# Optimization experiments

Hardware: AMD Instinct MI355X
Metric: run time of the kernel (lower is better)

## Reference

```python
import jax, jax.numpy as jnp
import numpy as np

KH, KW = 3, 3
PAD, STRIDE = 1, 1
KD = 3  # depth kernel extent; extended with one zero slice -> 4 indices


def _unfold(x, pad, stride):
    # x: (B, C, H, W) -> (B, C, KH*KW, oH, oW), patches ordered row-major like F.unfold
    B, C, H, W = x.shape
    xp = jnp.pad(x, ((0, 0), (0, 0), (pad, pad), (pad, pad)))
    oH = (H + 2 * pad - KH) // stride + 1
    oW = (W + 2 * pad - KW) // stride + 1
    pats = [xp[:, :, i:i + (oH - 1) * stride + 1:stride, j:j + (oW - 1) * stride + 1:stride]
            for i in range(KH) for j in range(KW)]
    return jnp.stack(pats, axis=2)


def setup_inputs() -> dict:
    key = jax.random.key(0)
    k1, k2, k3 = jax.random.split(key, 3)
    features = jax.random.normal(k1, (4, 16, 512, 512), dtype=jnp.float32)
    depth = jax.random.randint(k2, (4, 512, 512), 0, 8, dtype=jnp.int32)
    weight = jax.random.normal(k3, (32, 16, 3, 3, 3), dtype=jnp.float32) * 0.05
    return {"features": features, "depth": depth, "weight": weight}


def reference(features, depth, weight):
    oC, iC = weight.shape[0], weight.shape[1]
    # unfolded input patches: (B, iC, 9, oH, oW)
    patches = _unfold(features, PAD, STRIDE)
    # unfolded depth: (B, 9, oH, oW); padding fills with depth 0 (matches F.unfold)
    dpat = _unfold(depth[:, None, :, :].astype(jnp.int32), PAD, STRIDE)[:, 0]
    center = dpat[:, KH * KW // 2][:, None]  # (B, 1, oH, oW)
    diff = dpat - center
    # diff < -1 or diff >= 1 -> select appended zero slice (index 3); else diff+1
    idx = jnp.where((diff < -1) | (diff >= 1), 3, diff + 1)  # (B, 9, oH, oW) in [0, 3]
    onehot = jax.nn.one_hot(idx, KD + 1, dtype=features.dtype)  # (B, 9, oH, oW, 4)
    # extended weight with zero depth-slice: (oC, iC, 4, 9)
    ext_w = jnp.concatenate([weight, jnp.zeros_like(weight[:, :, :1])], axis=2)
    ext_w = ext_w.reshape(oC, iC, KD + 1, KH * KW)
    # per-pixel depth-gated 3x3x3 conv (bias is never added in the original op)
    out = jnp.einsum('oidk,bkhwd,bikhw->bohw', ext_w, onehot, patches)
    return out
```

## Files before the change

kernel.cpp:

```cpp
#include <hip/hip_runtime.h>
#include <hip/hip_bf16.h>


#define IC 16
#define OC 32
#define Hh 512
#define Ww 512
#define HW (Hh * Ww)
#define TW 256
#define TR 2
#define NT 4
#define SENTu 0x1000
#define PY  514
#define PXF 514
#define PXD 516
#define FTP_BYTES (4ull * PY * PXF * IC * 2)

typedef __attribute__((ext_vector_type(8))) short short8;
typedef __attribute__((ext_vector_type(4))) float float4v;
typedef __attribute__((ext_vector_type(2))) unsigned int uint2v;
typedef __attribute__((ext_vector_type(4))) unsigned int uint4v;

__device__ __forceinline__ unsigned short f2bf(float x) {
    unsigned u = __float_as_uint(x);
    unsigned r = u + 0x7FFFu + ((u >> 16) & 1u);
    return (unsigned short)(r >> 16);
}
__device__ __forceinline__ unsigned packbf(float a, float b) {
    union { __hip_bfloat162 h2; unsigned u; } cv;
    cv.h2 = __float22bfloat162_rn(make_float2(a, b));
    return cv.u;
}
__device__ __forceinline__ void gl16(const void* g, void* l) {
    __builtin_amdgcn_global_load_lds(
        (const __attribute__((address_space(1))) unsigned int*)g,
        (__attribute__((address_space(3))) unsigned int*)l, 16, 0, 0);
}
__device__ __forceinline__ void gl4(const void* g, void* l) {
    __builtin_amdgcn_global_load_lds(
        (const __attribute__((address_space(1))) unsigned int*)g,
        (__attribute__((address_space(3))) unsigned int*)l, 4, 0, 0);
}

__global__ void prep_weights(const float* __restrict__ wgt,
                             unsigned short* __restrict__ wsA) {
    int e = blockIdx.x * 256 + threadIdx.x;
    if (e >= 9 * 2 * 64 * 8) return;
    int j    = e & 7;
    int lane = (e >> 3) & 63;
    int mt   = (e >> 9) & 1;
    int c    = e >> 10;
    int oc = mt * 16 + (lane & 15);
    int kk = ((lane >> 4) << 3) + j;
    wsA[e] = f2bf(wgt[oc * 432 + (kk >> 1) * 27 + (kk & 1) * 9 + c]);
}

__global__ __launch_bounds__(256) void prep_feat(const float* __restrict__ feat,
                                                 unsigned short* __restrict__ ftp) {
    const int e  = blockIdx.x * 256 + threadIdx.x;
    const int xq = e & 127;
    const int y  = (e >> 7) & 511;
    const int b  = e >> 16;
    float4v v[16];
    const float* fb = feat + ((size_t)(b * IC) << 18) + (y << 9) + (xq << 2);
#pragma unroll
    for (int ic = 0; ic < IC; ++ic)
        v[ic] = *(const float4v*)(fb + ((size_t)ic << 18));
#pragma unroll
    for (int i = 0; i < 4; ++i) {
        const int xp = (xq << 2) + i + 1;
        const int q  = (xp >> 2) & 3;
        unsigned pk[8];
#pragma unroll
        for (int j = 0; j < 8; ++j)
            pk[j] = packbf(v[2 * j][i], v[2 * j + 1][i]);
        uint2v c0 = {pk[0], pk[1]}, c1 = {pk[2], pk[3]},
               c2 = {pk[4], pk[5]}, c3 = {pk[6], pk[7]};
        if (q & 1) { uint2v t = c0; c0 = c1; c1 = t; t = c2; c2 = c3; c3 = t; }
        if (q & 2) { uint2v t = c0; c0 = c2; c2 = t; t = c1; c1 = c3; c3 = t; }
        uint4v* dst = (uint4v*)(ftp + (((size_t)b * PY + (y + 1)) * PXF + xp) * 16);
        dst[0] = (uint4v){c0.x, c0.y, c1.x, c1.y};
        dst[1] = (uint4v){c2.x, c2.y, c3.x, c3.y};
    }
}

__global__ __launch_bounds__(256) void prep_depth(const int* __restrict__ depth,
                                                  unsigned short* __restrict__ dpad) {
    const int e = blockIdx.x * 256 + threadIdx.x;
    if (e >= 4 * PY * PXD) return;
    const int xp = e % PXD;
    const int yb = e / PXD;
    const int yp = yb % PY;
    const int b  = yb / PY;
    unsigned short v = (unsigned short)SENTu;
    const int xi = xp - 1, yi = yp - 1;
    if ((unsigned)xi < (unsigned)Ww && (unsigned)yi < (unsigned)Hh)
        v = (unsigned short)depth[(b << 18) + (yi << 9) + xi];
    dpad[e] = v;
}

__global__ __launch_bounds__(512, 2) void depconv_main(
    const unsigned short* __restrict__ ftp,
    const unsigned short* __restrict__ dpad,
    const unsigned short* __restrict__ wsA,
    float* __restrict__ out)
{
    __shared__ alignas(16) unsigned short ftile[2][TR + 2][258][16];
    __shared__ alignas(16) unsigned short dtile[2][TR + 2][260];

    const int tid = threadIdx.x;
    const int bid = blockIdx.x;
    const int wg  = (bid & 7) * 64 + (bid >> 3);
    const int t0  = wg * NT;

    const int lane = tid & 63;
    const int wv   = tid >> 6;
    const int g    = lane >> 4;
    const int n    = lane & 15;
    const int rr   = wv >> 2;
    const int xoff = (wv & 3) * 64;
    const int qs   = lane >> 4;
    const int oc0  = lane & 15;

    short8 wfrag[9][2];
    {
        const short8* ap = (const short8*)wsA;
#pragma unroll
        for (int c = 0; c < 9; ++c) {
            wfrag[c][0] = ap[(c * 2 + 0) * 64 + lane];
            wfrag[c][1] = ap[(c * 2 + 1) * 64 + lane];
        }
    }

    auto stageF = [&](int p, int tt) {
        const int b = tt >> 9, rowblk = (tt >> 1) & 255, colblk = tt & 1;
        const int h0 = rowblk * TR, wstart = colblk * TW;
        const char* gbase = (const char*)(ftp + (((size_t)b * PY + h0) * PXF + wstart) * 16);
#pragma unroll
        for (int r = 0; r < TR + 2; ++r) {
            const char* rg = gbase + (size_t)r * (PXF * 32);
            char* lr = (char*)&ftile[p][r][0][0];
            gl16(rg + tid * 16,      lr + wv * 1024);
            gl16(rg + 64 + tid * 16, lr + 64 + wv * 1024);
        }
    };
    auto stageD = [&](int p, int tt) {
        const int b = tt >> 9, rowblk = (tt >> 1) & 255, colblk = tt & 1;
        const int h0 = rowblk * TR, wstart = colblk * TW;
        const char* gb = (const char*)(dpad + ((size_t)b * PY + h0) * PXD + wstart);
        char* lb = (char*)&dtile[p][0][0];
#pragma unroll
        for (int pass = 0; pass < 2; ++pass) {
            const unsigned off = pass ? 32u : 0u;
            const unsigned d   = off + tid * 4;
            const unsigned row = d / 520u;
            const unsigned col = d - row * 520u;
            gl4(gb + (size_t)row * (PXD * 2) + col, lb + off + wv * 256);
        }
    };

    auto compute = [&](int p, int tt) {
        const int b = tt >> 9, rowblk = (tt >> 1) & 255, colblk = tt & 1;
        const int h0 = rowblk * TR, wstart = colblk * TW;
        const int h = h0 + rr;
        float* opb0 = out + ((size_t)(b * OC + oc0) << 18) + ((size_t)h << 9);
#pragma unroll 1
        for (int it = 0; it < 4; ++it) {
            const int xb = xoff + it * 16 + n;
            const int dc = (int)dtile[p][rr + 1][xb + 1];
            float4v acc0 = {0.f, 0.f, 0.f, 0.f};
            float4v acc1 = {0.f, 0.f, 0.f, 0.f};
#pragma unroll
            for (int t = 0; t < 9; ++t) {
                const int kh = t / 3, kw = t % 3;
                const int px = xb + kw;
                unsigned mm;
                if (t == 4) {
                    mm = 0xffff0000u;
                } else {
                    const int diff = (int)dtile[p][rr + kh][px] - dc;
                    mm = (diff == 0) ? 0xffff0000u : ((diff == -1) ? 0x0000ffffu : 0u);
                }
                const int slot = (g ^ ((px >> 2) & 3)) << 2;
                const uint2v pr = *(const uint2v*)(&ftile[p][rr + kh][px][slot]);
                union { short8 s; unsigned u[4]; } bf;
                bf.u[0] = __builtin_amdgcn_perm(0u, pr.x, 0x01000100u) & mm;
                bf.u[1] = __builtin_amdgcn_perm(0u, pr.x, 0x03020302u) & mm;
                bf.u[2] = __builtin_amdgcn_perm(0u, pr.y, 0x01000100u) & mm;
                bf.u[3] = __builtin_amdgcn_perm(0u, pr.y, 0x03020302u) & mm;

                acc0 = __builtin_amdgcn_mfma_f32_16x16x32_bf16(bf.s, wfrag[t][0], acc0, 0, 0, 0);
                acc1 = __builtin_amdgcn_mfma_f32_16x16x32_bf16(bf.s, wfrag[t][1], acc1, 0, 0, 0);
            }
            const int w16 = wstart + xoff + it * 16;
            float* op = opb0 + (w16 + 4 * qs);
            *(float4v*)op                      = acc0;
            *(float4v*)(op + ((size_t)16 << 18)) = acc1;
        }
    };

    stageF(0, t0);
    stageD(0, t0);
    __syncthreads();
#pragma unroll 1
    for (int i = 0; i < NT; ++i) {
        const int p = i & 1;
        if (i + 1 < NT) {
            stageF(p ^ 1, t0 + i + 1);
            stageD(p ^ 1, t0 + i + 1);
        }
        compute(p, t0 + i);
        __syncthreads();
    }
}

extern "C" void kernel_launch(void* const* d_in, const int* in_sizes, int n_in,
                              void* d_out, int out_size, void* d_ws, size_t ws_size,
                              hipStream_t stream) {
    const float* feat  = (const float*)d_in[0];
    const int*   depth = (const int*)d_in[1];
    const float* wgt   = (const float*)d_in[2];
    float* out = (float*)d_out;

    unsigned short* wsA  = (unsigned short*)d_ws;
    unsigned short* ftp  = (unsigned short*)((char*)d_ws + 32768);
    unsigned short* dpad = (unsigned short*)((char*)d_ws + 32768 + FTP_BYTES);

    prep_weights<<<36, 256, 0, stream>>>(wgt, wsA);
    prep_feat<<<1024, 256, 0, stream>>>(feat, ftp);
    prep_depth<<<(4 * PY * PXD + 255) / 256, 256, 0, stream>>>(depth, dpad);
    depconv_main<<<512, 512, 0, stream>>>(ftp, dpad, wsA, out);
}
```

Baseline: 256.3 us.

## Give each wave private LDS buffers with waitcnt pipelining; merge weight and depth prep

The main conv kernel now has each wave own a private double-buffered LDS strip (4 rows by 64+2 columns). Waves prefetch their next x-group with global_load_lds and wait with explicit vmcnt counters instead of block-wide __syncthreads. The grid shrinks to 256 blocks at occupancy 1, and each wave processes four 64-wide column groups of a row pair. The weight and depth prep kernels are merged into one launch to cut launch overhead. The change trades inter-wave halo sharing, which means more redundant global loads per tile, and the lower occupancy for removing block barriers.

```diff
diff --git a/kernel.cpp b/kernel.cpp
--- a/kernel.cpp
+++ b/kernel.cpp
@@ -7,14 +7,14 @@
 #define Hh 512
 #define Ww 512
 #define HW (Hh * Ww)
-#define TW 256
-#define TR 2
-#define NT 4
 #define SENTu 0x1000
 #define PY  514
 #define PXF 514
 #define PXD 516
 #define FTP_BYTES (4ull * PY * PXF * IC * 2)
+#define WTW 64
+#define FROWB 2112
+#define DROWB 256
 
 typedef __attribute__((ext_vector_type(8))) short short8;
 typedef __attribute__((ext_vector_type(4))) float float4v;
@@ -42,17 +42,34 @@
         (__attribute__((address_space(3))) unsigned int*)l, 4, 0, 0);
 }
 
-__global__ void prep_weights(const float* __restrict__ wgt,
-                             unsigned short* __restrict__ wsA) {
-    int e = blockIdx.x * 256 + threadIdx.x;
-    if (e >= 9 * 2 * 64 * 8) return;
-    int j    = e & 7;
-    int lane = (e >> 3) & 63;
-    int mt   = (e >> 9) & 1;
-    int c    = e >> 10;
-    int oc = mt * 16 + (lane & 15);
-    int kk = ((lane >> 4) << 3) + j;
-    wsA[e] = f2bf(wgt[oc * 432 + (kk >> 1) * 27 + (kk & 1) * 9 + c]);
+__global__ __launch_bounds__(256) void prep_misc(const float* __restrict__ wgt,
+                                                 const int* __restrict__ depth,
+                                                 unsigned short* __restrict__ wsA,
+                                                 unsigned short* __restrict__ dpad) {
+    const int bid = blockIdx.x;
+    if (bid < 36) {
+        int e = bid * 256 + threadIdx.x;
+        if (e >= 9 * 2 * 64 * 8) return;
+        int j    = e & 7;
+        int lane = (e >> 3) & 63;
+        int mt   = (e >> 9) & 1;
+        int c    = e >> 10;
+        int oc = mt * 16 + (lane & 15);
+        int kk = ((lane >> 4) << 3) + j;
+        wsA[e] = f2bf(wgt[oc * 432 + (kk >> 1) * 27 + (kk & 1) * 9 + c]);
+    } else {
+        int e = (bid - 36) * 256 + threadIdx.x;
+        if (e >= 4 * PY * PXD) return;
+        const int xp = e % PXD;
+        const int yb = e / PXD;
+        const int yp = yb % PY;
+        const int b  = yb / PY;
+        unsigned short v = (unsigned short)SENTu;
+        const int xi = xp - 1, yi = yp - 1;
+        if ((unsigned)xi < (unsigned)Ww && (unsigned)yi < (unsigned)Hh)
+            v = (unsigned short)depth[(b << 18) + (yi << 9) + xi];
+        dpad[e] = v;
+    }
 }
 
 __global__ __launch_bounds__(256) void prep_feat(const float* __restrict__ feat,
@@ -84,43 +101,29 @@
     }
 }
 
-__global__ __launch_bounds__(256) void prep_depth(const int* __restrict__ depth,
-                                                  unsigned short* __restrict__ dpad) {
-    const int e = blockIdx.x * 256 + threadIdx.x;
-    if (e >= 4 * PY * PXD) return;
-    const int xp = e % PXD;
-    const int yb = e / PXD;
-    const int yp = yb % PY;
-    const int b  = yb / PY;
-    unsigned short v = (unsigned short)SENTu;
-    const int xi = xp - 1, yi = yp - 1;
-    if ((unsigned)xi < (unsigned)Ww && (unsigned)yi < (unsigned)Hh)
-        v = (unsigned short)depth[(b << 18) + (yi << 9) + xi];
-    dpad[e] = v;
-}
-
-__global__ __launch_bounds__(512, 2) void depconv_main(
+__global__ __launch_bounds__(512, 1) void depconv_main(
     const unsigned short* __restrict__ ftp,
     const unsigned short* __restrict__ dpad,
     const unsigned short* __restrict__ wsA,
     float* __restrict__ out)
 {
-    __shared__ alignas(16) unsigned short ftile[2][TR + 2][258][16];
-    __shared__ alignas(16) unsigned short dtile[2][TR + 2][260];
-
-    const int tid = threadIdx.x;
-    const int bid = blockIdx.x;
-    const int wg  = (bid & 7) * 64 + (bid >> 3);
-    const int t0  = wg * NT;
-
+    __shared__ alignas(16) char fbuf[8][2][4 * FROWB];
+    __shared__ alignas(16) char dbuf[8][2][4 * DROWB];
+
+    const int tid  = threadIdx.x;
     const int lane = tid & 63;
     const int wv   = tid >> 6;
-    const int g    = lane >> 4;
-    const int n    = lane & 15;
-    const int rr   = wv >> 2;
-    const int xoff = (wv & 3) * 64;
-    const int qs   = lane >> 4;
-    const int oc0  = lane & 15;
+    const int bid  = blockIdx.x;
+    const int wgb  = (bid & 7) * 32 + (bid >> 3);
+    const int widG = wgb * 8 + wv;
+    const int rp   = widG >> 1;
+    const int b    = rp >> 8;
+    const int rowpair = rp & 255;
+    const int xg0  = (widG & 1) * 4;
+    const int h0p  = rowpair * 2;
+
+    const int g = lane >> 4, n = lane & 15;
+    const int qs = lane >> 4, oc0 = lane & 15;
 
     short8 wfrag[9][2];
     {
@@ -132,86 +135,85 @@
         }
     }
 
-    auto stageF = [&](int p, int tt) {
-        const int b = tt >> 9, rowblk = (tt >> 1) & 255, colblk = tt & 1;
-        const int h0 = rowblk * TR, wstart = colblk * TW;
-        const char* gbase = (const char*)(ftp + (((size_t)b * PY + h0) * PXF + wstart) * 16);
-#pragma unroll
-        for (int r = 0; r < TR + 2; ++r) {
-            const char* rg = gbase + (size_t)r * (PXF * 32);
-            char* lr = (char*)&ftile[p][r][0][0];
-            gl16(rg + tid * 16,      lr + wv * 1024);
-            gl16(rg + 64 + tid * 16, lr + 64 + wv * 1024);
+    char* fb[2] = {fbuf[wv][0], fbuf[wv][1]};
+    char* db[2] = {dbuf[wv][0], dbuf[wv][1]};
+
+    auto issue = [&](char* fB, char* dB, int xg) {
+        const int wx0 = xg * WTW;
+        const char* gf = (const char*)ftp + (((size_t)b * PY + h0p) * PXF + wx0) * 32;
+        const char* gd = (const char*)dpad + (((size_t)b * PY + h0p) * PXD + wx0) * 2;
+#pragma unroll
+        for (int r = 0; r < 4; ++r) {
+            const char* rg = gf + (size_t)r * (PXF * 32);
+            char* lr = fB + r * FROWB;
+            gl16(rg + lane * 16,        lr);
+            gl16(rg + 1024 + lane * 16, lr + 1024);
+            gl4 (rg + 1856 + lane * 4,  lr + 1856);
+            gl4 (gd + (size_t)r * (PXD * 2) + lane * 4, dB + r * DROWB);
         }
     };
-    auto stageD = [&](int p, int tt) {
-        const int b = tt >> 9, rowblk = (tt >> 1) & 255, colblk = tt & 1;
-        const int h0 = rowblk * TR, wstart = colblk * TW;
-        const char* gb = (const char*)(dpad + ((size_t)b * PY + h0) * PXD + wstart);
-        char* lb = (char*)&dtile[p][0][0];
-#pragma unroll
-        for (int pass = 0; pass < 2; ++pass) {
-            const unsigned off = pass ? 32u : 0u;
-            const unsigned d   = off + tid * 4;
-            const unsigned row = d / 520u;
-            const unsigned col = d - row * 520u;
-            gl4(gb + (size_t)row * (PXD * 2) + col, lb + off + wv * 256);
+
+    auto compute = [&](const char* fB, const char* dB, int xg) {
+        const int wx0 = xg * WTW;
+#pragma unroll
+        for (int ro = 0; ro < 2; ++ro) {
+            const int h = h0p + ro;
+            float* opb0 = out + ((size_t)(b * OC + oc0) << 18) + ((size_t)h << 9);
+#pragma unroll
+            for (int itx = 0; itx < 4; ++itx) {
+                const int xb = itx * 16 + n;
+                const int dc = (int)*(const unsigned short*)(dB + (ro + 1) * DROWB + (xb + 1) * 2);
+                float4v acc0 = {0.f, 0.f, 0.f, 0.f};
+                float4v acc1 = {0.f, 0.f, 0.f, 0.f};
+#pragma unroll
+                for (int t = 0; t < 9; ++t) {
+                    const int kh = t / 3, kw = t % 3;
+                    const int px = xb + kw;
+                    unsigned mm;
+                    if (t == 4) {
+                        mm = 0xffff0000u;
+                    } else {
+                        const int diff =
+                            (int)*(const unsigned short*)(dB + (ro + kh) * DROWB + px * 2) - dc;
+                        mm = (diff == 0) ? 0xffff0000u : ((diff == -1) ? 0x0000ffffu : 0u);
+                    }
+                    const int slot = (g ^ ((px >> 2) & 3)) << 3;
+                    const uint2v pr = *(const uint2v*)(fB + (ro + kh) * FROWB + px * 32 + slot);
+                    union { short8 s; unsigned u[4]; } bf;
+                    bf.u[0] = __builtin_amdgcn_perm(0u, pr.x, 0x01000100u) & mm;
+                    bf.u[1] = __builtin_amdgcn_perm(0u, pr.x, 0x03020302u) & mm;
+                    bf.u[2] = __builtin_amdgcn_perm(0u, pr.y, 0x01000100u) & mm;
+                    bf.u[3] = __builtin_amdgcn_perm(0u, pr.y, 0x03020302u) & mm;
+
+                    acc0 = __builtin_amdgcn_mfma_f32_16x16x32_bf16(bf.s, wfrag[t][0], acc0, 0, 0, 0);
+                    acc1 = __builtin_amdgcn_mfma_f32_16x16x32_bf16(bf.s, wfrag[t][1], acc1, 0, 0, 0);
+                }
+                float* op = opb0 + wx0 + itx * 16 + 4 * qs;
+                *(float4v*)op                        = acc0;
+                *(float4v*)(op + ((size_t)16 << 18)) = acc1;
+            }
         }
     };
 
-    auto compute = [&](int p, int tt) {
-        const int b = tt >> 9, rowblk = (tt >> 1) & 255, colblk = tt & 1;
-        const int h0 = rowblk * TR, wstart = colblk * TW;
-        const int h = h0 + rr;
-        float* opb0 = out + ((size_t)(b * OC + oc0) << 18) + ((size_t)h << 9);
-#pragma unroll 1
-        for (int it = 0; it < 4; ++it) {
-            const int xb = xoff + it * 16 + n;
-            const int dc = (int)dtile[p][rr + 1][xb + 1];
-            float4v acc0 = {0.f, 0.f, 0.f, 0.f};
-            float4v acc1 = {0.f, 0.f, 0.f, 0.f};
-#pragma unroll
-            for (int t = 0; t < 9; ++t) {
-                const int kh = t / 3, kw = t % 3;
-                const int px = xb + kw;
-                unsigned mm;
-                if (t == 4) {
-                    mm = 0xffff0000u;
-                } else {
-                    const int diff = (int)dtile[p][rr + kh][px] - dc;
-                    mm = (diff == 0) ? 0xffff0000u : ((diff == -1) ? 0x0000ffffu : 0u);
-                }
-                const int slot = (g ^ ((px >> 2) & 3)) << 2;
-                const uint2v pr = *(const uint2v*)(&ftile[p][rr + kh][px][slot]);
-                union { short8 s; unsigned u[4]; } bf;
-                bf.u[0] = __builtin_amdgcn_perm(0u, pr.x, 0x01000100u) & mm;
-                bf.u[1] = __builtin_amdgcn_perm(0u, pr.x, 0x03020302u) & mm;
-                bf.u[2] = __builtin_amdgcn_perm(0u, pr.y, 0x01000100u) & mm;
-                bf.u[3] = __builtin_amdgcn_perm(0u, pr.y, 0x03020302u) & mm;
-
-                acc0 = __builtin_amdgcn_mfma_f32_16x16x32_bf16(bf.s, wfrag[t][0], acc0, 0, 0, 0);
-                acc1 = __builtin_amdgcn_mfma_f32_16x16x32_bf16(bf.s, wfrag[t][1], acc1, 0, 0, 0);
-            }
-            const int w16 = wstart + xoff + it * 16;
-            float* op = opb0 + (w16 + 4 * qs);
-            *(float4v*)op                      = acc0;
-            *(float4v*)(op + ((size_t)16 << 18)) = acc1;
-        }
-    };
-
-    stageF(0, t0);
-    stageD(0, t0);
-    __syncthreads();
-#pragma unroll 1
-    for (int i = 0; i < NT; ++i) {
-        const int p = i & 1;
-        if (i + 1 < NT) {
-            stageF(p ^ 1, t0 + i + 1);
-            stageD(p ^ 1, t0 + i + 1);
-        }
-        compute(p, t0 + i);
-        __syncthreads();
-    }
+    issue(fb[0], db[0], xg0);
+    issue(fb[1], db[1], xg0 + 1);
+    asm volatile("s_waitcnt vmcnt(16)" ::: "memory");
+    __builtin_amdgcn_sched_barrier(0);
+    compute(fb[0], db[0], xg0);
+
+    issue(fb[0], db[0], xg0 + 2);
+    asm volatile("s_waitcnt vmcnt(16)" ::: "memory");
+    __builtin_amdgcn_sched_barrier(0);
+    compute(fb[1], db[1], xg0 + 1);
+
+    issue(fb[1], db[1], xg0 + 3);
+    asm volatile("s_waitcnt vmcnt(16)" ::: "memory");
+    __builtin_amdgcn_sched_barrier(0);
+    compute(fb[0], db[0], xg0 + 2);
+
+    asm volatile("s_waitcnt vmcnt(0)" ::: "memory");
+    __builtin_amdgcn_sched_barrier(0);
+    compute(fb[1], db[1], xg0 + 3);
 }
 
 extern "C" void kernel_launch(void* const* d_in, const int* in_sizes, int n_in,
@@ -226,8 +228,8 @@
     unsigned short* ftp  = (unsigned short*)((char*)d_ws + 32768);
     unsigned short* dpad = (unsigned short*)((char*)d_ws + 32768 + FTP_BYTES);
 
-    prep_weights<<<36, 256, 0, stream>>>(wgt, wsA);
+    const int depth_blocks = (4 * PY * PXD + 255) / 256;
+    prep_misc<<<36 + depth_blocks, 256, 0, stream>>>(wgt, depth, wsA, dpad);
     prep_feat<<<1024, 256, 0, stream>>>(feat, ftp);
-    prep_depth<<<(4 * PY * PXD + 255) / 256, 256, 0, stream>>>(depth, dpad);
-    depconv_main<<<512, 512, 0, stream>>>(ftp, dpad, wsA, out);
-}
+    depconv_main<<<256, 512, 0, stream>>>(ftp, dpad, wsA, out);
+}
```

Result: faster. 230.4 us (-10.1%).
